# Performance work log

Hardware: AMD Instinct MI355X
Metric: run time of the kernel (lower is better)

## Reference

```python
import jax, jax.numpy as jnp
import numpy as np

B, NPTS, H, O, L, PDIM, CDIM = 16, 20000, 128, 4, 6, 8, 3
K = 3  # number of learnable sine terms in Rowdy activation


def setup_inputs() -> dict:
    key = jax.random.key(0)
    ks = jax.random.split(key, 12)
    sc = lambda fan: 1.0 / np.sqrt(fan)
    return {
        "coords": jax.random.normal(ks[0], (B, NPTS, CDIM), dtype=jnp.float32),
        "sdf": jax.random.normal(ks[1], (B, NPTS, 1), dtype=jnp.float32),
        "params": jax.random.normal(ks[2], (B, PDIM), dtype=jnp.float32),
        # branch MLP: PDIM -> H (xL hidden) -> H*O
        "branch_W0": jax.random.normal(ks[3], (PDIM, H)) * sc(PDIM),
        "branch_Wr": jax.random.normal(ks[4], (L - 1, H, H)) * sc(H),
        "branch_b": jnp.zeros((L, H)),
        "branch_Wout": jax.random.normal(ks[5], (H, H * O)) * sc(H),
        "branch_bout": jnp.zeros((H * O,)),
        # trunk MLP: (CDIM+1) -> H (xL) with Rowdy activations
        "trunk_W0": jax.random.normal(ks[6], (CDIM + 1, H)) * sc(CDIM + 1),
        "trunk_Wr": jax.random.normal(ks[7], (L - 1, H, H)) * sc(H),
        "trunk_b": jnp.zeros((L, H)),
        "rowdy_a": 0.1 * jax.random.normal(ks[8], (L, K, H)),
        "final_W": jax.random.normal(ks[9], (H, H)) * sc(H),
        "final_b": jnp.zeros((H,)),
    }


def _rowdy(z, a):
    # Rowdy activation: tanh(z) + sum_k a_k * sin(k*z); a: (K, H)
    out = jnp.tanh(z)
    for k in range(a.shape[0]):
        out = out + a[k] * jnp.sin((k + 1.0) * z)
    return out


def reference(coords, sdf, params, branch_W0, branch_Wr, branch_b,
              branch_Wout, branch_bout, trunk_W0, trunk_Wr, trunk_b,
              rowdy_a, final_W, final_b):
    # ---- branch tower (records post-activation hiddens) ----
    h = jnp.tanh(params @ branch_W0 + branch_b[0])        # (B, H)
    hiddens = [h]
    for i in range(1, L):
        h = jnp.tanh(h @ branch_Wr[i - 1] + branch_b[i])
        hiddens.append(h)
    branch_out = h @ branch_Wout + branch_bout             # (B, H*O)
    # cumulative skip sums S_i = sum_{j<=i} hidden_j
    S = [hiddens[0]]
    for i in range(1, L):
        S.append(hiddens[i] + S[-1])
    # ---- trunk tower with fusion by accumulated branch features ----
    x = jnp.concatenate([coords, sdf], axis=-1)            # (B, NPTS, CDIM+1)
    for i in range(L):
        W = trunk_W0 if i == 0 else trunk_Wr[i - 1]
        x = _rowdy(x @ W + trunk_b[i], rowdy_a[i])         # (B, NPTS, H)
        x = x * S[i][:, None, :]                           # broadcast multiply
    YL = x @ final_W + final_b                             # (B, NPTS, H)
    ZL = branch_out.reshape(B, O, H)
    # sum(ZL * YL, -1) as batched contraction over H
    return jnp.einsum('boh,bnh->bno', ZL, YL)              # (B, NPTS, O)
```

## Files before the change

### kernel.cpp

```cpp
#include <hip/hip_runtime.h>
#include <hip/hip_bf16.h>
#include <stdint.h>

#define B_    16
#define NPTS_ 20000
#define H_    128
#define O_    4
#define L_    6
#define PDIM_ 8
#define K_    3

#define PTS_PER_WAVE 16
#define NTILES (NPTS_ / PTS_PER_WAVE)
#define NBLOCKS (B_ * NTILES / 4)

typedef __attribute__((ext_vector_type(8))) short short8;
typedef __attribute__((ext_vector_type(4))) float f32x4;
typedef __attribute__((ext_vector_type(2))) uint32_t u32x2;
typedef __attribute__((ext_vector_type(4))) uint32_t u32x4;

#define XSL(lam) ((uint32_t)(((lam)*16) ^ (((((lam)>>3)&3))<<4)))

__device__ __forceinline__ uint32_t cvt_pk_bf16(float a, float b) {
    uint32_t d;
    asm("v_cvt_pk_bf16_f32 %0, %1, %2" : "=v"(d) : "v"(a), "v"(b));
    return d;
}
__device__ __forceinline__ float bf2f(uint16_t h) {
    return __uint_as_float(((uint32_t)h) << 16);
}
__device__ __forceinline__ uint16_t f2bf(float x) {
    uint32_t u = __float_as_uint(x);
    uint32_t r = u + 0x7FFFu + ((u >> 16) & 1u);
    return (uint16_t)(r >> 16);
}
__device__ __forceinline__ short8 mk8(uint32_t a, uint32_t b, uint32_t c, uint32_t d) {
    u32x4 t = (u32x4){a, b, c, d};
    return __builtin_bit_cast(short8, t);
}
__device__ __forceinline__ float bperm_f(int byteaddr, float v) {
    return __int_as_float(__builtin_amdgcn_ds_bpermute(byteaddr, __float_as_int(v)));
}

__device__ __forceinline__ float rowdy_cf(float z, float S, float mS,
                                          float A0, float A1, float A2) {
    float e, s1, c1;
    float zl = z * 2.8853900817779268f;
    asm("v_exp_f32 %0, %1" : "=v"(e) : "v"(zl));
    float r = __builtin_amdgcn_rcpf(e + 1.f);
    float acc = fmaf(mS, r, S);
    float zs = z * 0.15915494309189535f;
    asm("v_sin_f32 %0, %1" : "=v"(s1) : "v"(zs));
    asm("v_cos_f32 %0, %1" : "=v"(c1) : "v"(zs));
    acc = fmaf(A0, s1, acc);
    acc = fmaf(A1, s1 * c1, acc);
    float t = s1 * s1;
    acc = fmaf(A2 * s1, fmaf(t, -4.f, 3.f), acc);
    return acc;
}

__device__ __forceinline__ void act_pack4_cf(const f32x4& v,
    const float4& S4, const float4& mS4, const float4& A0,
    const float4& A1, const float4& A2, u32x2& hi, u32x2& lo) {
    float x0 = rowdy_cf(v[0], S4.x, mS4.x, A0.x, A1.x, A2.x);
    float x1 = rowdy_cf(v[1], S4.y, mS4.y, A0.y, A1.y, A2.y);
    float x2 = rowdy_cf(v[2], S4.z, mS4.z, A0.z, A1.z, A2.z);
    float x3 = rowdy_cf(v[3], S4.w, mS4.w, A0.w, A1.w, A2.w);
    uint32_t d0 = cvt_pk_bf16(x0, x1);
    uint32_t d1 = cvt_pk_bf16(x2, x3);
    float r0 = x0 - __uint_as_float(d0 << 16);
    float r1 = x1 - __uint_as_float(d0 & 0xFFFF0000u);
    float r2 = x2 - __uint_as_float(d1 << 16);
    float r3 = x3 - __uint_as_float(d1 & 0xFFFF0000u);
    hi = (u32x2){d0, d1};
    lo = (u32x2){cvt_pk_bf16(r0, r1), cvt_pk_bf16(r2, r3)};
}

__global__ void prep_branch(
    const float* __restrict__ tWr,
    const float* __restrict__ params,
    const float* __restrict__ bW0, const float* __restrict__ bWr,
    const float* __restrict__ bb,  const float* __restrict__ bWout,
    const float* __restrict__ bbout,
    const float* __restrict__ fW,  const float* __restrict__ fb,
    const float* __restrict__ ra,
    uint16_t* __restrict__ WfH, uint16_t* __restrict__ WfL,
    float* __restrict__ CF, float* __restrict__ M, float* __restrict__ c0)
{
    const int blk = blockIdx.x;
    if (blk < 40) {
        const int layer = blk >> 3;
        const int JF    = blk & 7;
        const int t     = threadIdx.x;
        const int ks    = t >> 6;
        const int ln    = t & 63;
        const int j     = JF * 16 + (ln & 15);
        const int kbase = ks * 32 + (ln >> 4) * 8;
        uint16_t hi[8], lo[8];
        #pragma unroll
        for (int e = 0; e < 8; ++e) {
            float w = tWr[((size_t)layer * H_ + kbase + e) * H_ + j];
            uint16_t h = f2bf(w);
            hi[e] = h;
            lo[e] = f2bf(w - bf2f(h));
        }
        size_t dst = ((size_t)((layer * 8 + JF) * 4 + ks) * 64 + ln) * 8;
        #pragma unroll
        for (int e = 0; e < 8; ++e) { WfH[dst + e] = hi[e]; WfL[dst + e] = lo[e]; }
        return;
    }

    const int b = blk - 40;
    const int j = threadIdx.x & 127;
    __shared__ float h[H_];
    __shared__ float zl[O_][H_];

    float z = bb[j];
    #pragma unroll
    for (int k = 0; k < PDIM_; ++k)
        z = fmaf(params[b * PDIM_ + k], bW0[k * H_ + j], z);
    float hv = tanhf(z);
    float srun = hv;
    h[j] = hv;
    {
        float* cf = CF + (size_t)(0 * B_ + b) * 4 * H_;
        cf[0 * H_ + j] = srun;
        cf[1 * H_ + j] = ra[(0 * K_ + 0) * H_ + j] * srun;
        cf[2 * H_ + j] = 2.f * ra[(0 * K_ + 1) * H_ + j] * srun;
        cf[3 * H_ + j] = ra[(0 * K_ + 2) * H_ + j] * srun;
    }

    for (int i = 1; i < L_; ++i) {
        __syncthreads();
        const float* W = bWr + (size_t)(i - 1) * H_ * H_;
        float zz = bb[i * H_ + j];
        for (int k = 0; k < H_; ++k)
            zz = fmaf(h[k], W[k * H_ + j], zz);
        __syncthreads();
        hv = tanhf(zz);
        h[j] = hv;
        srun += hv;
        float* cf = CF + (size_t)(i * B_ + b) * 4 * H_;
        cf[0 * H_ + j] = srun;
        cf[1 * H_ + j] = ra[(i * K_ + 0) * H_ + j] * srun;
        cf[2 * H_ + j] = 2.f * ra[(i * K_ + 1) * H_ + j] * srun;
        cf[3 * H_ + j] = ra[(i * K_ + 2) * H_ + j] * srun;
    }
    __syncthreads();

    #pragma unroll
    for (int o = 0; o < O_; ++o) {
        float acc = bbout[o * H_ + j];
        for (int k = 0; k < H_; ++k)
            acc = fmaf(h[k], bWout[(size_t)k * (H_ * O_) + o * H_ + j], acc);
        zl[o][j] = acc;
    }
    __syncthreads();

    float m[O_] = {0.f, 0.f, 0.f, 0.f};
    for (int hh = 0; hh < H_; ++hh) {
        float w = fW[j * H_ + hh];
        #pragma unroll
        for (int o = 0; o < O_; ++o)
            m[o] = fmaf(w, zl[o][hh], m[o]);
    }
    #pragma unroll
    for (int o = 0; o < O_; ++o)
        M[((size_t)b * H_ + j) * O_ + o] = m[o];

    if (j < O_) {
        float acc = 0.f;
        for (int hh = 0; hh < H_; ++hh)
            acc = fmaf(fb[hh], zl[j][hh], acc);
        c0[b * O_ + j] = acc;
    }
}

__global__ __launch_bounds__(256, 4) void trunk_mfma(
    const float* __restrict__ coords, const float* __restrict__ sdf,
    const float* __restrict__ tW0,    const float* __restrict__ tb,
    const float* __restrict__ CF,     const float* __restrict__ M,
    const float* __restrict__ c0,
    const uint16_t* __restrict__ WfH, const uint16_t* __restrict__ WfL,
    float* __restrict__ out)
{
    __shared__ __align__(16) uint8_t XPK[4][8192];

    const int t   = threadIdx.x;
    const int wv  = t >> 6;
    const int l   = t & 63;
    const int gid = blockIdx.x * 4 + wv;
    const int b    = gid / NTILES;
    const int tile = gid % NTILES;
    const int p0   = tile * PTS_PER_WAVE;
    const int m    = l >> 4;
    const int p15  = l & 15;
    const int j4b  = m * 4;

    uint8_t* lb = &XPK[wv][0];
    uint8_t* pW = lb + XSL(l);
    const int lamA = ((l & 16) << 1) | p15;
    uint8_t* pA = lb + (uint32_t)((m >> 1) * 1024) + XSL(lamA);
    uint8_t* pB = lb + (uint32_t)((m >> 1) * 1024) + XSL(lamA + 16);

    {
        const size_t gp = (size_t)b * NPTS_ + p0 + p15;
        float in0 = coords[gp * 3 + 0], in1 = coords[gp * 3 + 1];
        float in2 = coords[gp * 3 + 2], in3 = sdf[gp];
        const float* cf0 = CF + (size_t)b * 4 * H_;
        #pragma unroll
        for (int JF = 0; JF < 8; ++JF) {
            const int j4 = JF * 16 + j4b;
            float4 w0 = *(const float4*)(tW0 + 0 * H_ + j4);
            float4 w1 = *(const float4*)(tW0 + 1 * H_ + j4);
            float4 w2 = *(const float4*)(tW0 + 2 * H_ + j4);
            float4 w3 = *(const float4*)(tW0 + 3 * H_ + j4);
            float4 bv = *(const float4*)(tb + j4);
            f32x4 zv;
            zv[0] = fmaf(in3, w3.x, fmaf(in2, w2.x, fmaf(in1, w1.x, fmaf(in0, w0.x, bv.x))));
            zv[1] = fmaf(in3, w3.y, fmaf(in2, w2.y, fmaf(in1, w1.y, fmaf(in0, w0.y, bv.y))));
            zv[2] = fmaf(in3, w3.z, fmaf(in2, w2.z, fmaf(in1, w1.z, fmaf(in0, w0.z, bv.z))));
            zv[3] = fmaf(in3, w3.w, fmaf(in2, w2.w, fmaf(in1, w1.w, fmaf(in0, w0.w, bv.w))));
            float4 S4 = *(const float4*)(cf0 + 0 * H_ + j4);
            float4 A0 = *(const float4*)(cf0 + 1 * H_ + j4);
            float4 A1 = *(const float4*)(cf0 + 2 * H_ + j4);
            float4 A2 = *(const float4*)(cf0 + 3 * H_ + j4);
            float4 mS4 = make_float4(-2.f * S4.x, -2.f * S4.y, -2.f * S4.z, -2.f * S4.w);
            u32x2 hi, lo;
            act_pack4_cf(zv, S4, mS4, A0, A1, A2, hi, lo);
            *(u32x4*)(pW + JF * 1024) = (u32x4){hi[0], hi[1], lo[0], lo[1]};
        }
    }

    const uint16_t* WH = WfH;
    const uint16_t* WL = WfL;
    #pragma unroll 1
    for (int layer = 1; layer <= 5; ++layer) {
        f32x4 acc[8];
        #pragma unroll
        for (int JF = 0; JF < 8; ++JF) {
            float4 bv = *(const float4*)(tb + layer * H_ + JF * 16 + j4b);
            acc[JF] = (f32x4){bv.x, bv.y, bv.z, bv.w};
        }
        #pragma unroll
        for (int ks = 0; ks < 4; ++ks) {
            u32x4 RA = *(const u32x4*)(pA + ks * 2048);
            u32x4 RB = *(const u32x4*)(pB + ks * 2048);
            short8 bH = mk8(RA.x, RA.y, RB.x, RB.y);
            short8 bL = mk8(RA.z, RA.w, RB.z, RB.w);
            #pragma unroll
            for (int JF = 0; JF < 8; ++JF) {
                const size_t off = (size_t)((JF * 4 + ks) * 512) + l * 8;
                short8 aH = *(const short8*)(WH + off);
                short8 aL = *(const short8*)(WL + off);
                acc[JF] = __builtin_amdgcn_mfma_f32_16x16x32_bf16(aH, bH, acc[JF], 0, 0, 0);
                acc[JF] = __builtin_amdgcn_mfma_f32_16x16x32_bf16(aH, bL, acc[JF], 0, 0, 0);
                acc[JF] = __builtin_amdgcn_mfma_f32_16x16x32_bf16(aL, bH, acc[JF], 0, 0, 0);
            }
        }
        const float* cf = CF + (size_t)(layer * B_ + b) * 4 * H_;
        #pragma unroll
        for (int JF = 0; JF < 8; ++JF) {
            const int j4 = JF * 16 + j4b;
            float4 S4 = *(const float4*)(cf + 0 * H_ + j4);
            float4 A0 = *(const float4*)(cf + 1 * H_ + j4);
            float4 A1 = *(const float4*)(cf + 2 * H_ + j4);
            float4 A2 = *(const float4*)(cf + 3 * H_ + j4);
            float4 mS4 = make_float4(-2.f * S4.x, -2.f * S4.y, -2.f * S4.z, -2.f * S4.w);
            u32x2 hi, lo;
            act_pack4_cf(acc[JF], S4, mS4, A0, A1, A2, hi, lo);
            *(u32x4*)(pW + JF * 1024) = (u32x4){hi[0], hi[1], lo[0], lo[1]};
        }
        WH += 8 * 2048;
        WL += 8 * 2048;
    }

    {
        f32x4 part = (f32x4){0.f, 0.f, 0.f, 0.f};
        const float* Mb = M + (size_t)b * H_ * O_;
        #pragma unroll
        for (int ks = 0; ks < 4; ++ks) {
            u32x4 RA = *(const u32x4*)(pA + ks * 2048);
            u32x4 RB = *(const u32x4*)(pB + ks * 2048);
            const int kb = ks * 32 + m * 8;
            uint32_t hw[4] = {RA.x, RA.y, RB.x, RB.y};
            uint32_t lw[4] = {RA.z, RA.w, RB.z, RB.w};
            #pragma unroll
            for (int q = 0; q < 4; ++q) {
                float xe = __uint_as_float(hw[q] << 16) + __uint_as_float(lw[q] << 16);
                float xo = __uint_as_float(hw[q] & 0xFFFF0000u) + __uint_as_float(lw[q] & 0xFFFF0000u);
                float4 Me = *(const float4*)(Mb + (size_t)(kb + 2 * q) * O_);
                float4 Mo = *(const float4*)(Mb + (size_t)(kb + 2 * q + 1) * O_);
                part[0] = fmaf(xe, Me.x, part[0]); part[0] = fmaf(xo, Mo.x, part[0]);
                part[1] = fmaf(xe, Me.y, part[1]); part[1] = fmaf(xo, Mo.y, part[1]);
                part[2] = fmaf(xe, Me.z, part[2]); part[2] = fmaf(xo, Mo.z, part[2]);
                part[3] = fmaf(xe, Me.w, part[3]); part[3] = fmaf(xo, Mo.w, part[3]);
            }
        }
        const int a16 = (l ^ 16) << 2;
        const int a32 = (l ^ 32) << 2;
        #pragma unroll
        for (int i = 0; i < 4; ++i) {
            float v = part[i];
            v += bperm_f(a16, v);
            v += bperm_f(a32, v);
            part[i] = v;
        }
        float4 cv = *(const float4*)(c0 + b * O_);
        if (l < 16) {
            float4 o4 = make_float4(part[0] + cv.x, part[1] + cv.y,
                                    part[2] + cv.z, part[3] + cv.w);
            *(float4*)(out + ((size_t)b * NPTS_ + p0 + l) * O_) = o4;
        }
    }
}

extern "C" void kernel_launch(void* const* d_in, const int* in_sizes, int n_in,
                              void* d_out, int out_size, void* d_ws, size_t ws_size,
                              hipStream_t stream) {
    const float* coords  = (const float*)d_in[0];
    const float* sdf     = (const float*)d_in[1];
    const float* params  = (const float*)d_in[2];
    const float* bW0     = (const float*)d_in[3];
    const float* bWr     = (const float*)d_in[4];
    const float* bb      = (const float*)d_in[5];
    const float* bWout   = (const float*)d_in[6];
    const float* bbout   = (const float*)d_in[7];
    const float* tW0     = (const float*)d_in[8];
    const float* tWr     = (const float*)d_in[9];
    const float* tb      = (const float*)d_in[10];
    const float* ra      = (const float*)d_in[11];
    const float* fW      = (const float*)d_in[12];
    const float* fb      = (const float*)d_in[13];
    float* out = (float*)d_out;

    float* CF = (float*)d_ws;
    float* M  = CF + (size_t)L_ * B_ * 4 * H_;
    float* c0 = M + (size_t)B_ * H_ * O_;
    uint16_t* WfH = (uint16_t*)(c0 + B_ * O_);
    uint16_t* WfL = WfH + (size_t)(L_ - 1) * H_ * H_;

    prep_branch<<<dim3(40 + B_), dim3(256), 0, stream>>>(
        tWr, params, bW0, bWr, bb, bWout, bbout, fW, fb, ra,
        WfH, WfL, CF, M, c0);
    trunk_mfma<<<dim3(NBLOCKS), dim3(256), 0, stream>>>(
        coords, sdf, tW0, tb, CF, M, c0, WfH, WfL, out);
}
```

Measured before the change: 476.6 us.

## Process two 16-point groups per wave to reuse weight fragments across MFMAs

Each wave now handles 32 points instead of 16, running two accumulator sets so every loaded weight fragment (aH/aL) feeds six MFMAs instead of three. The first group's packed activations are kept in registers while the second group's activations sit in the per-wave LDS buffer, so no extra shared memory is needed. This halves global/L2 weight traffic per point but raises register pressure, and the launch-bounds occupancy hint drops from 4 to 3 blocks, with half as many blocks in the grid.

Result: slower. 504.3 us (+5.8%).

```diff
diff --git a/kernel.cpp b/kernel.cpp
--- a/kernel.cpp
+++ b/kernel.cpp
@@ -10,7 +10,7 @@
 #define PDIM_ 8
 #define K_    3
 
-#define PTS_PER_WAVE 16
+#define PTS_PER_WAVE 32
 #define NTILES (NPTS_ / PTS_PER_WAVE)
 #define NBLOCKS (B_ * NTILES / 4)
 
@@ -176,7 +176,7 @@
     }
 }
 
-__global__ __launch_bounds__(256, 4) void trunk_mfma(
+__global__ __launch_bounds__(256, 3) void trunk_mfma(
     const float* __restrict__ coords, const float* __restrict__ sdf,
     const float* __restrict__ tW0,    const float* __restrict__ tb,
     const float* __restrict__ CF,     const float* __restrict__ M,
@@ -203,32 +203,44 @@
     uint8_t* pA = lb + (uint32_t)((m >> 1) * 1024) + XSL(lamA);
     uint8_t* pB = lb + (uint32_t)((m >> 1) * 1024) + XSL(lamA + 16);
 
+    u32x4 RA0[4], RB0[4];
+
     {
-        const size_t gp = (size_t)b * NPTS_ + p0 + p15;
-        float in0 = coords[gp * 3 + 0], in1 = coords[gp * 3 + 1];
-        float in2 = coords[gp * 3 + 2], in3 = sdf[gp];
         const float* cf0 = CF + (size_t)b * 4 * H_;
-        #pragma unroll
-        for (int JF = 0; JF < 8; ++JF) {
-            const int j4 = JF * 16 + j4b;
-            float4 w0 = *(const float4*)(tW0 + 0 * H_ + j4);
-            float4 w1 = *(const float4*)(tW0 + 1 * H_ + j4);
-            float4 w2 = *(const float4*)(tW0 + 2 * H_ + j4);
-            float4 w3 = *(const float4*)(tW0 + 3 * H_ + j4);
-            float4 bv = *(const float4*)(tb + j4);
-            f32x4 zv;
-            zv[0] = fmaf(in3, w3.x, fmaf(in2, w2.x, fmaf(in1, w1.x, fmaf(in0, w0.x, bv.x))));
-            zv[1] = fmaf(in3, w3.y, fmaf(in2, w2.y, fmaf(in1, w1.y, fmaf(in0, w0.y, bv.y))));
-            zv[2] = fmaf(in3, w3.z, fmaf(in2, w2.z, fmaf(in1, w1.z, fmaf(in0, w0.z, bv.z))));
-            zv[3] = fmaf(in3, w3.w, fmaf(in2, w2.w, fmaf(in1, w1.w, fmaf(in0, w0.w, bv.w))));
-            float4 S4 = *(const float4*)(cf0 + 0 * H_ + j4);
-            float4 A0 = *(const float4*)(cf0 + 1 * H_ + j4);
-            float4 A1 = *(const float4*)(cf0 + 2 * H_ + j4);
-            float4 A2 = *(const float4*)(cf0 + 3 * H_ + j4);
-            float4 mS4 = make_float4(-2.f * S4.x, -2.f * S4.y, -2.f * S4.z, -2.f * S4.w);
-            u32x2 hi, lo;
-            act_pack4_cf(zv, S4, mS4, A0, A1, A2, hi, lo);
-            *(u32x4*)(pW + JF * 1024) = (u32x4){hi[0], hi[1], lo[0], lo[1]};
+        #pragma unroll 1
+        for (int pf = 0; pf < 2; ++pf) {
+            const size_t gp = (size_t)b * NPTS_ + p0 + pf * 16 + p15;
+            float in0 = coords[gp * 3 + 0], in1 = coords[gp * 3 + 1];
+            float in2 = coords[gp * 3 + 2], in3 = sdf[gp];
+            #pragma unroll
+            for (int JF = 0; JF < 8; ++JF) {
+                const int j4 = JF * 16 + j4b;
+                float4 w0 = *(const float4*)(tW0 + 0 * H_ + j4);
+                float4 w1 = *(const float4*)(tW0 + 1 * H_ + j4);
+                float4 w2 = *(const float4*)(tW0 + 2 * H_ + j4);
+                float4 w3 = *(const float4*)(tW0 + 3 * H_ + j4);
+                float4 bv = *(const float4*)(tb + j4);
+                f32x4 zv;
+                zv[0] = fmaf(in3, w3.x, fmaf(in2, w2.x, fmaf(in1, w1.x, fmaf(in0, w0.x, bv.x))));
+                zv[1] = fmaf(in3, w3.y, fmaf(in2, w2.y, fmaf(in1, w1.y, fmaf(in0, w0.y, bv.y))));
+                zv[2] = fmaf(in3, w3.z, fmaf(in2, w2.z, fmaf(in1, w1.z, fmaf(in0, w0.z, bv.z))));
+                zv[3] = fmaf(in3, w3.w, fmaf(in2, w2.w, fmaf(in1, w1.w, fmaf(in0, w0.w, bv.w))));
+                float4 S4 = *(const float4*)(cf0 + 0 * H_ + j4);
+                float4 A0 = *(const float4*)(cf0 + 1 * H_ + j4);
+                float4 A1 = *(const float4*)(cf0 + 2 * H_ + j4);
+                float4 A2 = *(const float4*)(cf0 + 3 * H_ + j4);
+                float4 mS4 = make_float4(-2.f * S4.x, -2.f * S4.y, -2.f * S4.z, -2.f * S4.w);
+                u32x2 hi, lo;
+                act_pack4_cf(zv, S4, mS4, A0, A1, A2, hi, lo);
+                *(u32x4*)(pW + JF * 1024) = (u32x4){hi[0], hi[1], lo[0], lo[1]};
+            }
+            if (pf == 0) {
+                #pragma unroll
+                for (int ks = 0; ks < 4; ++ks) {
+                    RA0[ks] = *(const u32x4*)(pA + ks * 2048);
+                    RB0[ks] = *(const u32x4*)(pB + ks * 2048);
+                }
+            }
         }
     }
 
@@ -236,29 +248,37 @@
     const uint16_t* WL = WfL;
     #pragma unroll 1
     for (int layer = 1; layer <= 5; ++layer) {
-        f32x4 acc[8];
+        f32x4 acc0[8], acc1[8];
         #pragma unroll
         for (int JF = 0; JF < 8; ++JF) {
             float4 bv = *(const float4*)(tb + layer * H_ + JF * 16 + j4b);
-            acc[JF] = (f32x4){bv.x, bv.y, bv.z, bv.w};
+            acc0[JF] = (f32x4){bv.x, bv.y, bv.z, bv.w};
+            acc1[JF] = acc0[JF];
         }
         #pragma unroll
         for (int ks = 0; ks < 4; ++ks) {
-            u32x4 RA = *(const u32x4*)(pA + ks * 2048);
-            u32x4 RB = *(const u32x4*)(pB + ks * 2048);
-            short8 bH = mk8(RA.x, RA.y, RB.x, RB.y);
-            short8 bL = mk8(RA.z, RA.w, RB.z, RB.w);
+            u32x4 RA1 = *(const u32x4*)(pA + ks * 2048);
+            u32x4 RB1 = *(const u32x4*)(pB + ks * 2048);
+            short8 bH0 = mk8(RA0[ks].x, RA0[ks].y, RB0[ks].x, RB0[ks].y);
+            short8 bL0 = mk8(RA0[ks].z, RA0[ks].w, RB0[ks].z, RB0[ks].w);
+            short8 bH1 = mk8(RA1.x, RA1.y, RB1.x, RB1.y);
+            short8 bL1 = mk8(RA1.z, RA1.w, RB1.z, RB1.w);
             #pragma unroll
             for (int JF = 0; JF < 8; ++JF) {
                 const size_t off = (size_t)((JF * 4 + ks) * 512) + l * 8;
                 short8 aH = *(const short8*)(WH + off);
                 short8 aL = *(const short8*)(WL + off);
-                acc[JF] = __builtin_amdgcn_mfma_f32_16x16x32_bf16(aH, bH, acc[JF], 0, 0, 0);
-                acc[JF] = __builtin_amdgcn_mfma_f32_16x16x32_bf16(aH, bL, acc[JF], 0, 0, 0);
-                acc[JF] = __builtin_amdgcn_mfma_f32_16x16x32_bf16(aL, bH, acc[JF], 0, 0, 0);
-            }
-        }
+                acc0[JF] = __builtin_amdgcn_mfma_f32_16x16x32_bf16(aH, bH0, acc0[JF], 0, 0, 0);
+                acc0[JF] = __builtin_amdgcn_mfma_f32_16x16x32_bf16(aH, bL0, acc0[JF], 0, 0, 0);
+                acc0[JF] = __builtin_amdgcn_mfma_f32_16x16x32_bf16(aL, bH0, acc0[JF], 0, 0, 0);
+                acc1[JF] = __builtin_amdgcn_mfma_f32_16x16x32_bf16(aH, bH1, acc1[JF], 0, 0, 0);
+                acc1[JF] = __builtin_amdgcn_mfma_f32_16x16x32_bf16(aH, bL1, acc1[JF], 0, 0, 0);
+                acc1[JF] = __builtin_amdgcn_mfma_f32_16x16x32_bf16(aL, bH1, acc1[JF], 0, 0, 0);
+            }
+        }
+
         const float* cf = CF + (size_t)(layer * B_ + b) * 4 * H_;
+        u32x4 xp1[8];
         #pragma unroll
         for (int JF = 0; JF < 8; ++JF) {
             const int j4 = JF * 16 + j4b;
@@ -268,49 +288,67 @@
             float4 A2 = *(const float4*)(cf + 3 * H_ + j4);
             float4 mS4 = make_float4(-2.f * S4.x, -2.f * S4.y, -2.f * S4.z, -2.f * S4.w);
             u32x2 hi, lo;
-            act_pack4_cf(acc[JF], S4, mS4, A0, A1, A2, hi, lo);
+            act_pack4_cf(acc0[JF], S4, mS4, A0, A1, A2, hi, lo);
             *(u32x4*)(pW + JF * 1024) = (u32x4){hi[0], hi[1], lo[0], lo[1]};
-        }
+            act_pack4_cf(acc1[JF], S4, mS4, A0, A1, A2, hi, lo);
+            xp1[JF] = (u32x4){hi[0], hi[1], lo[0], lo[1]};
+        }
+        #pragma unroll
+        for (int ks = 0; ks < 4; ++ks) {
+            RA0[ks] = *(const u32x4*)(pA + ks * 2048);
+            RB0[ks] = *(const u32x4*)(pB + ks * 2048);
+        }
+        #pragma unroll
+        for (int JF = 0; JF < 8; ++JF)
+            *(u32x4*)(pW + JF * 1024) = xp1[JF];
+
         WH += 8 * 2048;
         WL += 8 * 2048;
     }
 
     {
-        f32x4 part = (f32x4){0.f, 0.f, 0.f, 0.f};
         const float* Mb = M + (size_t)b * H_ * O_;
-        #pragma unroll
-        for (int ks = 0; ks < 4; ++ks) {
-            u32x4 RA = *(const u32x4*)(pA + ks * 2048);
-            u32x4 RB = *(const u32x4*)(pB + ks * 2048);
-            const int kb = ks * 32 + m * 8;
-            uint32_t hw[4] = {RA.x, RA.y, RB.x, RB.y};
-            uint32_t lw[4] = {RA.z, RA.w, RB.z, RB.w};
-            #pragma unroll
-            for (int q = 0; q < 4; ++q) {
-                float xe = __uint_as_float(hw[q] << 16) + __uint_as_float(lw[q] << 16);
-                float xo = __uint_as_float(hw[q] & 0xFFFF0000u) + __uint_as_float(lw[q] & 0xFFFF0000u);
-                float4 Me = *(const float4*)(Mb + (size_t)(kb + 2 * q) * O_);
-                float4 Mo = *(const float4*)(Mb + (size_t)(kb + 2 * q + 1) * O_);
-                part[0] = fmaf(xe, Me.x, part[0]); part[0] = fmaf(xo, Mo.x, part[0]);
-                part[1] = fmaf(xe, Me.y, part[1]); part[1] = fmaf(xo, Mo.y, part[1]);
-                part[2] = fmaf(xe, Me.z, part[2]); part[2] = fmaf(xo, Mo.z, part[2]);
-                part[3] = fmaf(xe, Me.w, part[3]); part[3] = fmaf(xo, Mo.w, part[3]);
-            }
-        }
+        float4 cv = *(const float4*)(c0 + b * O_);
         const int a16 = (l ^ 16) << 2;
         const int a32 = (l ^ 32) << 2;
-        #pragma unroll
-        for (int i = 0; i < 4; ++i) {
-            float v = part[i];
-            v += bperm_f(a16, v);
-            v += bperm_f(a32, v);
-            part[i] = v;
-        }
-        float4 cv = *(const float4*)(c0 + b * O_);
-        if (l < 16) {
-            float4 o4 = make_float4(part[0] + cv.x, part[1] + cv.y,
-                                    part[2] + cv.z, part[3] + cv.w);
-            *(float4*)(out + ((size_t)b * NPTS_ + p0 + l) * O_) = o4;
+        #pragma unroll 1
+        for (int pf = 0; pf < 2; ++pf) {
+            f32x4 part = (f32x4){0.f, 0.f, 0.f, 0.f};
+            #pragma unroll
+            for (int ks = 0; ks < 4; ++ks) {
+                u32x4 RA, RB;
+                if (pf == 0) { RA = RA0[ks]; RB = RB0[ks]; }
+                else {
+                    RA = *(const u32x4*)(pA + ks * 2048);
+                    RB = *(const u32x4*)(pB + ks * 2048);
+                }
+                const int kb = ks * 32 + m * 8;
+                uint32_t hw[4] = {RA.x, RA.y, RB.x, RB.y};
+                uint32_t lw[4] = {RA.z, RA.w, RB.z, RB.w};
+                #pragma unroll
+                for (int q = 0; q < 4; ++q) {
+                    float xe = __uint_as_float(hw[q] << 16) + __uint_as_float(lw[q] << 16);
+                    float xo = __uint_as_float(hw[q] & 0xFFFF0000u) + __uint_as_float(lw[q] & 0xFFFF0000u);
+                    float4 Me = *(const float4*)(Mb + (size_t)(kb + 2 * q) * O_);
+                    float4 Mo = *(const float4*)(Mb + (size_t)(kb + 2 * q + 1) * O_);
+                    part[0] = fmaf(xe, Me.x, part[0]); part[0] = fmaf(xo, Mo.x, part[0]);
+                    part[1] = fmaf(xe, Me.y, part[1]); part[1] = fmaf(xo, Mo.y, part[1]);
+                    part[2] = fmaf(xe, Me.z, part[2]); part[2] = fmaf(xo, Mo.z, part[2]);
+                    part[3] = fmaf(xe, Me.w, part[3]); part[3] = fmaf(xo, Mo.w, part[3]);
+                }
+            }
+            #pragma unroll
+            for (int i = 0; i < 4; ++i) {
+                float v = part[i];
+                v += bperm_f(a16, v);
+                v += bperm_f(a32, v);
+                part[i] = v;
+            }
+            if (l < 16) {
+                float4 o4 = make_float4(part[0] + cv.x, part[1] + cv.y,
+                                        part[2] + cv.z, part[3] + cv.w);
+                *(float4*)(out + ((size_t)b * NPTS_ + p0 + pf * 16 + l) * O_) = o4;
+            }
         }
     }
 }
```
